# Optimization experiments

Hardware: AMD Instinct MI355X
Metric: run time of the kernel (lower is better)

The kernel has to match this reference:

```python
import jax, jax.numpy as jnp
import numpy as np

UNITS = 400    # LSTM cells per hidden layer
KATT = 10     # attention Gaussians
NCHARS = 73   # alphabet size
NMIX = 20     # bivariate GMM components


def _peephole_step(x, h, c, Wx, Wh, b, p):
    # p: [3, U] peephole weights (i, f, o)
    z = x @ Wx + h @ Wh + b                       # [B, 4U]
    zi, zf, zg, zo = jnp.split(z, 4, axis=-1)
    i = jax.nn.sigmoid(zi + p[0] * c)
    f = jax.nn.sigmoid(zf + p[1] * c)
    c_new = f * c + i * jnp.tanh(zg)
    o = jax.nn.sigmoid(zo + p[2] * c_new)
    return o * jnp.tanh(c_new), c_new


def _forward(input_strokes, char_onehot, char_mask,
             Wx0, Wh0, b0, p0, Wx1, Wh1, b1, p1, Wx2, Wh2, b2, p2,
             W_att, b_att, W_mdn, b_mdn):
    B, T, _ = input_strokes.shape
    Uc = char_onehot.shape[1]
    dt = input_strokes.dtype
    u = jnp.arange(Uc, dtype=dt)                  # character positions

    def step(carry, x_t):
        h1, c1, h2, c2, h3, c3, kappa, w = carry
        # layer 1: [stroke, window]
        h1, c1 = _peephole_step(jnp.concatenate([x_t, w], -1), h1, c1, Wx0, Wh0, b0, p0)
        # Graves soft-window attention from h1
        att = h1 @ W_att + b_att                  # [B, 3K]
        a_hat, b_hat, k_hat = jnp.split(att, 3, axis=-1)
        alpha = jnp.exp(a_hat)
        beta = jnp.exp(b_hat)
        kappa = kappa + jnp.exp(k_hat)            # [B, K] monotone position
        diff = kappa[:, :, None] - u[None, None, :]                   # [B, K, Uc]
        phi = jnp.sum(alpha[:, :, None] * jnp.exp(-beta[:, :, None] * diff * diff), axis=1)
        phi = phi * char_mask                     # [B, Uc] mask padded chars
        w = jnp.einsum('bu,buc->bc', phi, char_onehot)                # [B, NCHARS]
        # layers 2/3 with skip connections
        h2, c2 = _peephole_step(jnp.concatenate([x_t, w, h1], -1), h2, c2, Wx1, Wh1, b1, p1)
        h3, c3 = _peephole_step(jnp.concatenate([x_t, w, h2], -1), h3, c3, Wx2, Wh2, b2, p2)
        return (h1, c1, h2, c2, h3, c3, kappa, w), h3

    zh = jnp.zeros((B, UNITS), dt)
    carry0 = (zh, zh, zh, zh, zh, zh,
              jnp.zeros((B, KATT), dt), jnp.zeros((B, NCHARS), dt))
    _, hs = jax.lax.scan(step, carry0, input_strokes.transpose(1, 0, 2))
    outputs = hs.transpose(1, 0, 2)               # [B, T, UNITS]

    # mixture density head: 6*M + 1 outputs
    y = outputs @ W_mdn + b_mdn                   # [B, T, 6M+1]
    M = NMIX
    pi, mu1, mu2, s1, s2, rho, eos = jnp.split(
        y, [M, 2 * M, 3 * M, 4 * M, 5 * M, 6 * M], axis=-1)
    return jnp.concatenate([
        jax.nn.softmax(pi, axis=-1), mu1, mu2,
        jnp.exp(s1), jnp.exp(s2), jnp.tanh(rho), jax.nn.sigmoid(eos)], axis=-1)


def setup_inputs() -> dict:
    key = jax.random.key(0)
    ks = jax.random.split(key, 16)
    B, T, Uc = 32, 400, 50
    s = 0.1
    in0 = 3 + NCHARS                 # stroke + window
    in12 = 3 + NCHARS + UNITS        # stroke + window + skip h
    d = {
        'input_strokes': jax.random.normal(ks[0], (B, T, 3), jnp.float32),
        'input_chars': jax.random.randint(ks[1], (B, Uc), 0, NCHARS),
        'input_char_lens': jax.random.randint(ks[2], (B,), 10, Uc + 1),
        'Wx0': s * jax.random.normal(ks[3], (in0, 4 * UNITS), jnp.float32),
        'Wh0': s * jax.random.normal(ks[4], (UNITS, 4 * UNITS), jnp.float32),
        'b0': jnp.zeros((4 * UNITS,), jnp.float32),
        'p0': s * jax.random.normal(ks[5], (3, UNITS), jnp.float32),
        'Wx1': s * jax.random.normal(ks[6], (in12, 4 * UNITS), jnp.float32),
        'Wh1': s * jax.random.normal(ks[7], (UNITS, 4 * UNITS), jnp.float32),
        'b1': jnp.zeros((4 * UNITS,), jnp.float32),
        'p1': s * jax.random.normal(ks[8], (3, UNITS), jnp.float32),
        'Wx2': s * jax.random.normal(ks[9], (in12, 4 * UNITS), jnp.float32),
        'Wh2': s * jax.random.normal(ks[10], (UNITS, 4 * UNITS), jnp.float32),
        'b2': jnp.zeros((4 * UNITS,), jnp.float32),
        'p2': s * jax.random.normal(ks[11], (3, UNITS), jnp.float32),
        'W_att': s * jax.random.normal(ks[12], (UNITS, 3 * KATT), jnp.float32),
        'b_att': jnp.zeros((3 * KATT,), jnp.float32),
        'W_mdn': s * jax.random.normal(ks[13], (UNITS, 6 * NMIX + 1), jnp.float32),
        'b_mdn': jnp.zeros((6 * NMIX + 1,), jnp.float32),
    }
    return d


def reference(input_strokes, input_chars, input_char_lens,
              Wx0, Wh0, b0, p0, Wx1, Wh1, b1, p1, Wx2, Wh2, b2, p2,
              W_att, b_att, W_mdn, b_mdn):
    char_onehot = jax.nn.one_hot(input_chars, NCHARS, dtype=input_strokes.dtype)
    Uc = input_chars.shape[1]
    char_mask = (jnp.arange(Uc)[None, :] < input_char_lens[:, None]).astype(input_strokes.dtype)
    return _forward(input_strokes, char_onehot, char_mask,
                    Wx0, Wh0, b0, p0, Wx1, Wh1, b1, p1, Wx2, Wh2, b2, p2,
                    W_att, b_att, W_mdn, b_mdn)
```

## Files before the change

### kernel.cpp

```cpp
#include <hip/hip_runtime.h>


#define NATT   8
#define NBLK   208
#define NBLKC  200
#define NTHR   1024
#define TSTEPS 400
#define BATCH  32
#define UNITSN 400
#define NCHARS 73
#define UC     50
#define KTOT   2228
#define WSTR   2236
#define NGRP   8
#define NFLAG  32
#define NEPOCH 402

typedef unsigned int       u32;
typedef unsigned long long u64;

#define STATE_BYTES 4096
#define HSLOT     12832
#define H1_BYTE   4096
#define H2_BYTE   (H1_BYTE + TSTEPS * HSLOT * 4)
#define H3_BYTE   (H2_BYTE + TSTEPS * HSLOT * 4)
#define WSLOT     2368
#define WH_BYTE   (H3_BYTE + TSTEPS * HSLOT * 4)

__device__ __forceinline__ float sigf(float x)   { return 1.0f / (1.0f + __expf(-x)); }
__device__ __forceinline__ float tanhf_(float x) { return 1.0f - 2.0f / (1.0f + __expf(2.0f * x)); }

__device__ __forceinline__ float dot100(const float* __restrict__ w,
                                        const float* __restrict__ x) {
  const float4* wv = (const float4*)w;
  const float4* xv = (const float4*)x;
  float s0 = 0.f, s1 = 0.f, s2 = 0.f, s3 = 0.f;
#pragma unroll 5
  for (int i = 0; i < 25; ++i) {
    float4 a = wv[i], bb = xv[i];
    s0 = fmaf(a.x, bb.x, s0); s1 = fmaf(a.y, bb.y, s1);
    s2 = fmaf(a.z, bb.z, s2); s3 = fmaf(a.w, bb.w, s3);
  }
  return (s0 + s1) + (s2 + s3);
}

__device__ __forceinline__ void dot100x2(const float* __restrict__ wa,
                                         const float* __restrict__ wb,
                                         const float* __restrict__ x,
                                         float& ra, float& rb) {
  const float4* av = (const float4*)wa;
  const float4* bv = (const float4*)wb;
  const float4* xv = (const float4*)x;
  float a0 = 0.f, a1 = 0.f, a2 = 0.f, a3 = 0.f;
  float c0 = 0.f, c1 = 0.f, c2 = 0.f, c3 = 0.f;
#pragma unroll 5
  for (int i = 0; i < 25; ++i) {
    float4 xx = xv[i], aa = av[i], bb = bv[i];
    a0 = fmaf(aa.x, xx.x, a0); a1 = fmaf(aa.y, xx.y, a1);
    a2 = fmaf(aa.z, xx.z, a2); a3 = fmaf(aa.w, xx.w, a3);
    c0 = fmaf(bb.x, xx.x, c0); c1 = fmaf(bb.y, xx.y, c1);
    c2 = fmaf(bb.z, xx.z, c2); c3 = fmaf(bb.w, xx.w, c3);
  }
  ra += (a0 + a1) + (a2 + a3);
  rb += (c0 + c1) + (c2 + c3);
}

__device__ __forceinline__ void dotP3(const float* __restrict__ wA,
                                      const float* __restrict__ wB,
                                      const float* __restrict__ x2,
                                      const float* __restrict__ wC,
                                      const float* __restrict__ wD,
                                      const float* __restrict__ x1,
                                      const float* __restrict__ wE,
                                      const float* __restrict__ x3,
                                      float& r3, float& r2, float& r1) {
  const float4* Av = (const float4*)wA;
  const float4* Bv = (const float4*)wB;
  const float4* Cv = (const float4*)wC;
  const float4* Dv = (const float4*)wD;
  const float4* Ev = (const float4*)wE;
  const float4* x2v = (const float4*)x2;
  const float4* x1v = (const float4*)x1;
  const float4* x3v = (const float4*)x3;
  float sA0 = 0.f, sA1 = 0.f, sA2 = 0.f, sA3 = 0.f;
  float sB0 = 0.f, sB1 = 0.f, sB2 = 0.f, sB3 = 0.f;
  float sC0 = 0.f, sC1 = 0.f, sC2 = 0.f, sC3 = 0.f;
  float sD0 = 0.f, sD1 = 0.f, sD2 = 0.f, sD3 = 0.f;
  float sE0 = 0.f, sE1 = 0.f, sE2 = 0.f, sE3 = 0.f;
#pragma unroll 2
  for (int i = 0; i < 25; ++i) {
    float4 xa = x2v[i], xb = x1v[i], xc = x3v[i];
    float4 a = Av[i], bb = Bv[i], cc = Cv[i], d = Dv[i], e = Ev[i];
    sA0 = fmaf(a.x, xa.x, sA0);  sA1 = fmaf(a.y, xa.y, sA1);
    sA2 = fmaf(a.z, xa.z, sA2);  sA3 = fmaf(a.w, xa.w, sA3);
    sB0 = fmaf(bb.x, xa.x, sB0); sB1 = fmaf(bb.y, xa.y, sB1);
    sB2 = fmaf(bb.z, xa.z, sB2); sB3 = fmaf(bb.w, xa.w, sB3);
    sC0 = fmaf(cc.x, xb.x, sC0); sC1 = fmaf(cc.y, xb.y, sC1);
    sC2 = fmaf(cc.z, xb.z, sC2); sC3 = fmaf(cc.w, xb.w, sC3);
    sD0 = fmaf(d.x, xb.x, sD0);  sD1 = fmaf(d.y, xb.y, sD1);
    sD2 = fmaf(d.z, xb.z, sD2);  sD3 = fmaf(d.w, xb.w, sD3);
    sE0 = fmaf(e.x, xc.x, sE0);  sE1 = fmaf(e.y, xc.y, sE1);
    sE2 = fmaf(e.z, xc.z, sE2);  sE3 = fmaf(e.w, xc.w, sE3);
  }
  r3 += (sA0 + sA1) + (sA2 + sA3) + (sE0 + sE1) + (sE2 + sE3);
  r2 += (sB0 + sB1) + (sB2 + sB3) + (sC0 + sC1) + (sC2 + sC3);
  r1 += (sD0 + sD1) + (sD2 + sD3);
}

__device__ __forceinline__ void dot73x3(const float* __restrict__ w1,
                                        const float* __restrict__ w2,
                                        const float* __restrict__ w3,
                                        const float* __restrict__ x, int kq,
                                        float& r1, float& r2, float& r3) {
  int st = (kq == 0) ? 0 : 18 * kq + 1;
  int en = st + ((kq == 0) ? 19 : 18);
  float s1 = 0.f, s2 = 0.f, s3 = 0.f;
  for (int k = st; k < en; ++k) {
    float xv = x[k];
    s1 = fmaf(w1[k], xv, s1); s2 = fmaf(w2[k], xv, s2); s3 = fmaf(w3[k], xv, s3);
  }
  r1 += s1; r2 += s2; r3 += s3;
}

extern "C" __global__ void __launch_bounds__(NTHR)
__attribute__((amdgpu_waves_per_eu(4, 4)))
hand_kernel(const float* __restrict__ xs, const int* __restrict__ chars,
            const int* __restrict__ lens,
            const float* __restrict__ Wx0, const float* __restrict__ Wh0,
            const float* __restrict__ b0, const float* __restrict__ p0,
            const float* __restrict__ Wx1, const float* __restrict__ Wh1,
            const float* __restrict__ b1, const float* __restrict__ p1,
            const float* __restrict__ Wx2, const float* __restrict__ Wh2,
            const float* __restrict__ b2, const float* __restrict__ p2,
            const float* __restrict__ Watt, const float* __restrict__ batt,
            const float* __restrict__ Wmdn, const float* __restrict__ bmdn,
            float* __restrict__ dout, char* __restrict__ wsb) {
  const int blk = blockIdx.x;
  const int tid = threadIdx.x;
  const bool is_att = (blk < NATT);
  const int cblk = blk - NATT;

  __shared__ __align__(16) float wlw[8 * WSTR];
  __shared__ float zpart[NTHR], zpartB[NTHR];
  __shared__ float zbuf[256], zbufB[256];
  __shared__ float biasL[3][8];
  __shared__ float peepL[3][3][2];
  __shared__ float cstate[3][64];
  __shared__ int   bar_target;
  __shared__ float alphaL[40], betaL[40], kappaL[40];
  __shared__ float wlds[4 * NCHARS];
  __shared__ __align__(16) float wstg[BATCH * NCHARS + 12];

  int*   bar_i = (int*)wsb;
  int*   glob  = bar_i + 128;
  int*   wcnt  = bar_i + 192;
  float* h1h   = (float*)(wsb + H1_BYTE);
  float* h2h   = (float*)(wsb + H2_BYTE);
  float* h3h   = (float*)(wsb + H3_BYTE);
  float* whh   = (float*)(wsb + WH_BYTE);

  const int out = tid & 255;
  const int b   = out >> 3;
  const int c   = out & 7;
  const int kq  = tid >> 8;
  const int u0  = 2 * cblk;

  if (tid == 0) bar_target = 0;
  if (tid < 192) cstate[tid / 64][tid % 64] = 0.f;
  if (tid < 40) kappaL[tid] = 0.f;

  if (!is_att) {
    for (int idx = tid; idx < 8 * KTOT; idx += NTHR) {
      int cc = idx / KTOT, k = idx - cc * KTOT;
      int gcol = (cc & 3) * UNITSN + u0 + (cc >> 2);
      float v;
      if (k < 476)        v = (k < 76)  ? Wx0[(size_t)k * 1600 + gcol]
                                        : Wh0[(size_t)(k - 76) * 1600 + gcol];
      else if (k < 1352) { int q = k - 476;
                          v = (q < 476) ? Wx1[(size_t)q * 1600 + gcol]
                                        : Wh1[(size_t)(q - 476) * 1600 + gcol]; }
      else               { int q = k - 1352;
                          v = (q < 476) ? Wx2[(size_t)q * 1600 + gcol]
                                        : Wh2[(size_t)(q - 476) * 1600 + gcol]; }
      wlw[cc * WSTR + k] = v;
    }
    if (tid < 24) {
      int l = tid >> 3, cc = tid & 7;
      const float* bs = (l == 0) ? b0 : (l == 1) ? b1 : b2;
      biasL[l][cc] = bs[(cc & 3) * UNITSN + u0 + (cc >> 2)];
    }
    if (tid < 18) {
      int l = tid / 6, r = (tid % 6) >> 1, ul = tid & 1;
      const float* ps = (l == 0) ? p0 : (l == 1) ? p1 : p2;
      peepL[l][r][ul] = ps[r * UNITSN + u0 + ul];
    }
  } else {
    for (int i = tid; i < 12000; i += NTHR) wlw[i] = Watt[i];
  }
  __syncthreads();

  const float* Wc   = wlw + c * WSTR;
  float*       attp = wlw + 12000;

  auto gridbar = [&]() {
    __syncthreads();
    if (tid == 0) {
      int e = ++bar_target;
      int g = cblk & (NGRP - 1);
      const int gsz = NBLKC / NGRP;
      int a = __hip_atomic_fetch_add(bar_i + g * 16, 1, __ATOMIC_RELAXED, __HIP_MEMORY_SCOPE_AGENT);
      if (a + 1 == e * gsz) {
        int q = __hip_atomic_fetch_add(glob, 1, __ATOMIC_RELAXED, __HIP_MEMORY_SCOPE_AGENT);
        if (((q + 1) & (NGRP - 1)) == 0) {
          for (int f = 0; f < NFLAG; ++f)
            __hip_atomic_store(bar_i + 256 + f * 16, e, __ATOMIC_RELAXED, __HIP_MEMORY_SCOPE_AGENT);
        }
      }
      int* myflag = bar_i + 256 + (cblk & (NFLAG - 1)) * 16;
      while (__hip_atomic_load(myflag, __ATOMIC_RELAXED, __HIP_MEMORY_SCOPE_AGENT) < e)
        __builtin_amdgcn_s_sleep(2);
    }
    __syncthreads();
  };

  auto waitglob = [&](int e) {
    if (tid == 0) {
      int tgt = NGRP * e;
      while (__hip_atomic_load(glob, __ATOMIC_RELAXED, __HIP_MEMORY_SCOPE_AGENT) < tgt)
        __builtin_amdgcn_s_sleep(2);
    }
    __syncthreads();
  };

  auto gates = [&](int layer, const float* zb, int bb, float* hdst) {
    union { float f[2]; u64 v; } pk;
#pragma unroll
    for (int ul = 0; ul < 2; ++ul) {
      float zi = zb[bb * 8 + ul * 4 + 0], zf = zb[bb * 8 + ul * 4 + 1];
      float zg = zb[bb * 8 + ul * 4 + 2], zo = zb[bb * 8 + ul * 4 + 3];
      float cold = cstate[layer][ul * 32 + bb];
      float ig = sigf(zi + peepL[layer][0][ul] * cold);
      float fg = sigf(zf + peepL[layer][1][ul] * cold);
      float cn = fg * cold + ig * tanhf_(zg);
      float og = sigf(zo + peepL[layer][2][ul] * cn);
      cstate[layer][ul * 32 + bb] = cn;
      pk.f[ul] = og * tanhf_(cn);
    }
    __hip_atomic_store((u64*)(hdst + bb * UNITSN + u0), pk.v,
                       __ATOMIC_RELAXED, __HIP_MEMORY_SCOPE_AGENT);
  };

  auto finalize1 = [&](int layer, float acc, float* hdst) {
    zpart[tid] = acc;
    __syncthreads();
    if (tid < 256)
      zbuf[tid] = zpart[tid] + zpart[tid + 256] + zpart[tid + 512] + zpart[tid + 768]
                + biasL[layer][tid & 7];
    __syncthreads();
    if (tid < 256 && (tid & 7) == 0) gates(layer, zbuf, tid >> 3, hdst);
  };

  auto finalizeQ = [&](float a2v, float* h2dst, float a1v, float* h1dst, bool do1) {
    zpart[tid]  = a2v;
    zpartB[tid] = a1v;
    __syncthreads();
    if (tid < 256) {
      zbuf[tid]  = zpart[tid]  + zpart[tid + 256]  + zpart[tid + 512]  + zpart[tid + 768]
                 + biasL[1][tid & 7];
      zbufB[tid] = zpartB[tid] + zpartB[tid + 256] + zpartB[tid + 512] + zpartB[tid + 768]
                 + biasL[0][tid & 7];
    }
    __syncthreads();
    if (tid < 256 && (tid & 7) == 0) {
      gates(1, zbuf, tid >> 3, h2dst);
      if (do1) gates(0, zbufB, tid >> 3, h1dst);
    }
  };

  if (is_att) {
    const int bs0 = blk * 4;
    for (int t = 0; t < TSTEPS; ++t) {
      waitglob(t + 1);
      const float* h1g = h1h + (size_t)t * HSLOT;
      float* wdst = whh + (size_t)t * WSLOT + bs0 * NCHARS;
      for (int i = tid; i < 4 * NCHARS; i += NTHR) wlds[i] = 0.f;
      if (tid < 240) {
        int ks = tid / 30, r = tid - ks * 30;
        int bb2 = r / 15, jj2 = r - bb2 * 15;
        int j0 = 2 * jj2, j1 = j0 + 1;
        const float2* h0v = (const float2*)(h1g + (bs0 + 2 * bb2) * UNITSN + ks * 50);
        const float2* h1v = (const float2*)(h1g + (bs0 + 2 * bb2 + 1) * UNITSN + ks * 50);
        const float* wv = wlw + (ks * 50) * 30;
        float s00 = 0.f, s01 = 0.f, s10 = 0.f, s11 = 0.f;
#pragma unroll
        for (int kk = 0; kk < 25; ++kk) {
          float2 ha = h0v[kk], hb = h1v[kk];
          float wa0 = wv[(2 * kk) * 30 + j0],     wb0 = wv[(2 * kk) * 30 + j1];
          float wa1 = wv[(2 * kk + 1) * 30 + j0], wb1 = wv[(2 * kk + 1) * 30 + j1];
          s00 = fmaf(ha.x, wa0, s00); s01 = fmaf(ha.x, wb0, s01);
          s10 = fmaf(hb.x, wa0, s10); s11 = fmaf(hb.x, wb0, s11);
          s00 = fmaf(ha.y, wa1, s00); s01 = fmaf(ha.y, wb1, s01);
          s10 = fmaf(hb.y, wa1, s10); s11 = fmaf(hb.y, wb1, s11);
        }
        int b0i = 2 * bb2;
        attp[(b0i * 30 + j0) * 8 + ks] = s00;
        attp[(b0i * 30 + j1) * 8 + ks] = s01;
        attp[((b0i + 1) * 30 + j0) * 8 + ks] = s10;
        attp[((b0i + 1) * 30 + j1) * 8 + ks] = s11;
      }
      __syncthreads();
      if (tid < 40) {
        int bl = tid / 10, j = tid - bl * 10;
        float ah = batt[j], bh = batt[10 + j], kh = batt[20 + j];
#pragma unroll
        for (int s = 0; s < 8; ++s) {
          ah += attp[(bl * 30 + j) * 8 + s];
          bh += attp[(bl * 30 + 10 + j) * 8 + s];
          kh += attp[(bl * 30 + 20 + j) * 8 + s];
        }
        float kap = kappaL[tid] + __expf(kh);
        kappaL[tid] = kap;
        alphaL[tid] = __expf(ah);
        betaL[tid]  = __expf(bh);
      }
      __syncthreads();
      if (tid < 4 * UC) {
        int bl = tid / UC, u = tid - bl * UC;
        if (u < lens[bs0 + bl]) {
          float ph = 0.f;
#pragma unroll
          for (int j = 0; j < 10; ++j) {
            float d = kappaL[bl * 10 + j] - (float)u;
            ph = fmaf(alphaL[bl * 10 + j], __expf(-betaL[bl * 10 + j] * d * d), ph);
          }
          atomicAdd(&wlds[bl * NCHARS + chars[(bs0 + bl) * UC + u]], ph);
        }
      }
      __syncthreads();
      for (int i = tid; i < (4 * NCHARS) / 2; i += NTHR) {
        union { float f[2]; u64 v; } pk;
        pk.f[0] = wlds[2 * i]; pk.f[1] = wlds[2 * i + 1];
        __hip_atomic_store((u64*)(wdst + 2 * i), pk.v,
                           __ATOMIC_RELAXED, __HIP_MEMORY_SCOPE_AGENT);
      }
      __syncthreads();
      if (tid == 0)
        __hip_atomic_fetch_add(wcnt, 1, __ATOMIC_RELAXED, __HIP_MEMORY_SCOPE_AGENT);
    }
    waitglob(NEPOCH);
  }
  else {
    {
      float acc = 0.f;
      if (kq == 0) {
        const float* xr = xs + (size_t)b * TSTEPS * 3;
        acc = Wc[0] * xr[0] + Wc[1] * xr[1] + Wc[2] * xr[2];
      }
      finalize1(0, acc, h1h);
    }
    gridbar();

    float acc_z3 = 0.f;
    for (int t = 0; t < TSTEPS; ++t) {
      const float* h1t  = h1h + (size_t)t * HSLOT + b * UNITSN;
      const float* h2p  = h2h + (size_t)(t > 0 ? t - 1 : 0) * HSLOT + b * UNITSN;
      const float* h3pp = h3h + (size_t)(t > 1 ? t - 2 : 0) * HSLOT + b * UNITSN;
      const int o = kq * 100;
      float a3f = acc_z3, a2 = 0.f, a1 = 0.f;
      if (t >= 2) {
        dotP3(Wc + 1428 + o, Wc + 952 + o, h2p + o,
              Wc + 552 + o,  Wc + 76 + o,  h1t + o,
              Wc + 1828 + o, h3pp + o, a3f, a2, a1);
      } else if (t == 1) {
        dot100x2(Wc + 1428 + o, Wc + 952 + o, h2p + o, a3f, a2);
        dot100x2(Wc + 552 + o, Wc + 76 + o, h1t + o, a2, a1);
      } else {
        dot100x2(Wc + 552 + o, Wc + 76 + o, h1t + o, a2, a1);
      }
      if (kq == 0) {
        const float* xr = xs + ((size_t)b * TSTEPS + t) * 3;
        a2 += Wc[476] * xr[0] + Wc[477] * xr[1] + Wc[478] * xr[2];
        if (t < TSTEPS - 1)
          a1 += Wc[0] * xr[3] + Wc[1] * xr[4] + Wc[2] * xr[5];
      }
      if (t > 0) finalize1(2, a3f, h3h + (size_t)(t - 1) * HSLOT);
      if (tid == 0) {
        int tgt = NATT * (t + 1);
        while (__hip_atomic_load(wcnt, __ATOMIC_RELAXED, __HIP_MEMORY_SCOPE_AGENT) < tgt)
          __builtin_amdgcn_s_sleep(2);
      }
      __syncthreads();
      {
        const float4* wsrc = (const float4*)(whh + (size_t)t * WSLOT);
        for (int i = tid; i < (BATCH * NCHARS) / 4; i += NTHR)
          ((float4*)wstg)[i] = wsrc[i];
      }
      __syncthreads();
      bool do1 = (t < TSTEPS - 1);
      float q2 = a2, q1 = a1, z3n = 0.f;
      dot73x3(Wc + 479, Wc + 3, Wc + 1355, wstg + b * NCHARS, kq, q2, q1, z3n);
      if (kq == 0) {
        const float* xr = xs + ((size_t)b * TSTEPS + t) * 3;
        z3n += Wc[1352] * xr[0] + Wc[1353] * xr[1] + Wc[1354] * xr[2];
      }
      finalizeQ(q2, h2h + (size_t)t * HSLOT,
                q1, h1h + (size_t)(t + 1) * HSLOT, do1);
      acc_z3 = z3n;
      gridbar();
    }
    {
      const float* h2l  = h2h + (size_t)(TSTEPS - 1) * HSLOT + b * UNITSN;
      const float* h3ll = h3h + (size_t)(TSTEPS - 2) * HSLOT + b * UNITSN;
      float a3 = acc_z3 + dot100(Wc + 1428 + kq * 100, h2l + kq * 100)
                        + dot100(Wc + 1828 + kq * 100, h3ll + kq * 100);
      finalize1(2, a3, h3h + (size_t)(TSTEPS - 1) * HSLOT);
    }
    gridbar();
  }

  {
    int j = tid & 127, ks = tid >> 7;
    for (int i0 = 0; i0 < 64; i0 += 4) {
      float acc[4] = {0.f, 0.f, 0.f, 0.f};
      const float* hp[4];
      bool val[4];
      for (int r = 0; r < 4; ++r) {
        int row = blk + (i0 + r) * NBLK;
        val[r] = (row < 12800);
        hp[r] = val[r] ? (h3h + (size_t)(row % TSTEPS) * HSLOT + (row / TSTEPS) * UNITSN + ks * 50)
                       : h3h;
      }
      if (j < 121) {
        const float* wp = Wmdn + (size_t)(ks * 50) * 121 + j;
        for (int k = 0; k < 50; ++k) {
          float wv = wp[(size_t)k * 121];
#pragma unroll
          for (int r = 0; r < 4; ++r) acc[r] = fmaf(hp[r][k], wv, acc[r]);
        }
      }
      for (int r = 0; r < 4; ++r) {
        zpart[tid] = acc[r];
        __syncthreads();
        if (tid < 121) {
          float s = bmdn[tid];
#pragma unroll
          for (int m = 0; m < 8; ++m) s += zpart[tid + m * 128];
          zbuf[tid] = s;
        }
        __syncthreads();
        if (tid == 0) {
          float mx = zbuf[0];
          for (int q = 1; q < 20; ++q) mx = fmaxf(mx, zbuf[q]);
          float s = 0.f;
          for (int q = 0; q < 20; ++q) s += __expf(zbuf[q] - mx);
          zbuf[126] = mx;
          zbuf[127] = 1.f / s;
        }
        __syncthreads();
        if (val[r] && tid < 121) {
          int row = blk + (i0 + r) * NBLK;
          float y = zbuf[tid], o;
          if (tid < 20)       o = __expf(y - zbuf[126]) * zbuf[127];
          else if (tid < 60)  o = y;
          else if (tid < 100) o = __expf(y);
          else if (tid < 120) o = tanhf_(y);
          else                o = sigf(y);
          dout[(size_t)row * 121 + tid] = o;
        }
        __syncthreads();
      }
    }
  }
}

extern "C" void kernel_launch(void* const* d_in, const int* in_sizes, int n_in,
                              void* d_out, int out_size, void* d_ws, size_t ws_size,
                              hipStream_t stream) {
  const float* xs   = (const float*)d_in[0];
  const int*   chrs = (const int*)d_in[1];
  const int*   lens = (const int*)d_in[2];
  const float* Wx0  = (const float*)d_in[3];
  const float* Wh0  = (const float*)d_in[4];
  const float* b0   = (const float*)d_in[5];
  const float* p0   = (const float*)d_in[6];
  const float* Wx1  = (const float*)d_in[7];
  const float* Wh1  = (const float*)d_in[8];
  const float* b1   = (const float*)d_in[9];
  const float* p1   = (const float*)d_in[10];
  const float* Wx2  = (const float*)d_in[11];
  const float* Wh2  = (const float*)d_in[12];
  const float* b2   = (const float*)d_in[13];
  const float* p2   = (const float*)d_in[14];
  const float* Watt = (const float*)d_in[15];
  const float* batt = (const float*)d_in[16];
  const float* Wmdn = (const float*)d_in[17];
  const float* bmdn = (const float*)d_in[18];

  hipMemsetAsync(d_ws, 0, STATE_BYTES, stream);
  hipLaunchKernelGGL(hand_kernel, dim3(NBLK), dim3(NTHR), 0, stream,
                     xs, chrs, lens, Wx0, Wh0, b0, p0, Wx1, Wh1, b1, p1,
                     Wx2, Wh2, b2, p2, Watt, batt, Wmdn, bmdn,
                     (float*)d_out, (char*)d_ws);
}
```

Baseline: 7.138 ms.

## Spread LSTM recurrence across 400 compute blocks with one unit each

Doubles the compute blocks from 200 to 400 so each block owns one hidden unit (4 gate columns) instead of two. The K reduction is now split eight ways (52-wide slices) rather than four. The LDS weight footprint per block is halved, and waves_per_eu is raised to 8 so two blocks can share a CU. The intent is to shorten each block's serial per-step dot-product work in the latency-bound persistent recurrence. The cost is twice as many participants in every grid barrier, more fragmented per-unit h stores, and a deeper LDS partial-sum reduction.

```diff
diff --git a/kernel.cpp b/kernel.cpp
--- a/kernel.cpp
+++ b/kernel.cpp
@@ -2,8 +2,8 @@
 
 
 #define NATT   8
-#define NBLK   208
-#define NBLKC  200
+#define NBLKC  400
+#define NBLK   408
 #define NTHR   1024
 #define TSTEPS 400
 #define BATCH  32
@@ -30,13 +30,14 @@
 __device__ __forceinline__ float sigf(float x)   { return 1.0f / (1.0f + __expf(-x)); }
 __device__ __forceinline__ float tanhf_(float x) { return 1.0f - 2.0f / (1.0f + __expf(2.0f * x)); }
 
-__device__ __forceinline__ float dot100(const float* __restrict__ w,
-                                        const float* __restrict__ x) {
+template<int N4>
+__device__ __forceinline__ float dotX(const float* __restrict__ w,
+                                      const float* __restrict__ x) {
   const float4* wv = (const float4*)w;
   const float4* xv = (const float4*)x;
   float s0 = 0.f, s1 = 0.f, s2 = 0.f, s3 = 0.f;
-#pragma unroll 5
-  for (int i = 0; i < 25; ++i) {
+#pragma unroll
+  for (int i = 0; i < N4; ++i) {
     float4 a = wv[i], bb = xv[i];
     s0 = fmaf(a.x, bb.x, s0); s1 = fmaf(a.y, bb.y, s1);
     s2 = fmaf(a.z, bb.z, s2); s3 = fmaf(a.w, bb.w, s3);
@@ -44,17 +45,18 @@
   return (s0 + s1) + (s2 + s3);
 }
 
-__device__ __forceinline__ void dot100x2(const float* __restrict__ wa,
-                                         const float* __restrict__ wb,
-                                         const float* __restrict__ x,
-                                         float& ra, float& rb) {
+template<int N4>
+__device__ __forceinline__ void dotX2(const float* __restrict__ wa,
+                                      const float* __restrict__ wb,
+                                      const float* __restrict__ x,
+                                      float& ra, float& rb) {
   const float4* av = (const float4*)wa;
   const float4* bv = (const float4*)wb;
   const float4* xv = (const float4*)x;
   float a0 = 0.f, a1 = 0.f, a2 = 0.f, a3 = 0.f;
   float c0 = 0.f, c1 = 0.f, c2 = 0.f, c3 = 0.f;
-#pragma unroll 5
-  for (int i = 0; i < 25; ++i) {
+#pragma unroll
+  for (int i = 0; i < N4; ++i) {
     float4 xx = xv[i], aa = av[i], bb = bv[i];
     a0 = fmaf(aa.x, xx.x, a0); a1 = fmaf(aa.y, xx.y, a1);
     a2 = fmaf(aa.z, xx.z, a2); a3 = fmaf(aa.w, xx.w, a3);
@@ -65,6 +67,7 @@
   rb += (c0 + c1) + (c2 + c3);
 }
 
+template<int N4>
 __device__ __forceinline__ void dotP3(const float* __restrict__ wA,
                                       const float* __restrict__ wB,
                                       const float* __restrict__ x2,
@@ -88,7 +91,7 @@
   float sD0 = 0.f, sD1 = 0.f, sD2 = 0.f, sD3 = 0.f;
   float sE0 = 0.f, sE1 = 0.f, sE2 = 0.f, sE3 = 0.f;
 #pragma unroll 2
-  for (int i = 0; i < 25; ++i) {
+  for (int i = 0; i < N4; ++i) {
     float4 xa = x2v[i], xb = x1v[i], xc = x3v[i];
     float4 a = Av[i], bb = Bv[i], cc = Cv[i], d = Dv[i], e = Ev[i];
     sA0 = fmaf(a.x, xa.x, sA0);  sA1 = fmaf(a.y, xa.y, sA1);
@@ -112,8 +115,8 @@
                                         const float* __restrict__ w3,
                                         const float* __restrict__ x, int kq,
                                         float& r1, float& r2, float& r3) {
-  int st = (kq == 0) ? 0 : 18 * kq + 1;
-  int en = st + ((kq == 0) ? 19 : 18);
+  int st = kq * 9;
+  int en = st + ((kq == 7) ? 10 : 9);
   float s1 = 0.f, s2 = 0.f, s3 = 0.f;
   for (int k = st; k < en; ++k) {
     float xv = x[k];
@@ -123,7 +126,7 @@
 }
 
 extern "C" __global__ void __launch_bounds__(NTHR)
-__attribute__((amdgpu_waves_per_eu(4, 4)))
+__attribute__((amdgpu_waves_per_eu(8, 8)))
 hand_kernel(const float* __restrict__ xs, const int* __restrict__ chars,
             const int* __restrict__ lens,
             const float* __restrict__ Wx0, const float* __restrict__ Wh0,
@@ -140,12 +143,12 @@
   const bool is_att = (blk < NATT);
   const int cblk = blk - NATT;
 
-  __shared__ __align__(16) float wlw[8 * WSTR];
+  __shared__ __align__(16) float wlw[12960];
   __shared__ float zpart[NTHR], zpartB[NTHR];
-  __shared__ float zbuf[256], zbufB[256];
-  __shared__ float biasL[3][8];
-  __shared__ float peepL[3][3][2];
-  __shared__ float cstate[3][64];
+  __shared__ float zbuf[128], zbufB[128];
+  __shared__ float biasL[3][4];
+  __shared__ float peepL[3][3];
+  __shared__ float cstate[3][32];
   __shared__ int   bar_target;
   __shared__ float alphaL[40], betaL[40], kappaL[40];
   __shared__ float wlds[4 * NCHARS];
@@ -159,20 +162,21 @@
   float* h3h   = (float*)(wsb + H3_BYTE);
   float* whh   = (float*)(wsb + WH_BYTE);
 
-  const int out = tid & 255;
-  const int b   = out >> 3;
-  const int c   = out & 7;
-  const int kq  = tid >> 8;
-  const int u0  = 2 * cblk;
+  const int out = tid & 127;
+  const int b   = out >> 2;
+  const int c   = out & 3;
+  const int kq  = tid >> 7;
+  const int u0  = cblk;
+  const int ko  = kq * 52;
 
   if (tid == 0) bar_target = 0;
-  if (tid < 192) cstate[tid / 64][tid % 64] = 0.f;
+  if (tid < 96) cstate[tid / 32][tid % 32] = 0.f;
   if (tid < 40) kappaL[tid] = 0.f;
 
   if (!is_att) {
-    for (int idx = tid; idx < 8 * KTOT; idx += NTHR) {
+    for (int idx = tid; idx < 4 * KTOT; idx += NTHR) {
       int cc = idx / KTOT, k = idx - cc * KTOT;
-      int gcol = (cc & 3) * UNITSN + u0 + (cc >> 2);
+      int gcol = cc * UNITSN + u0;
       float v;
       if (k < 476)        v = (k < 76)  ? Wx0[(size_t)k * 1600 + gcol]
                                         : Wh0[(size_t)(k - 76) * 1600 + gcol];
@@ -184,15 +188,15 @@
                                         : Wh2[(size_t)(q - 476) * 1600 + gcol]; }
       wlw[cc * WSTR + k] = v;
     }
-    if (tid < 24) {
-      int l = tid >> 3, cc = tid & 7;
+    if (tid < 12) {
+      int l = tid >> 2, cc = tid & 3;
       const float* bs = (l == 0) ? b0 : (l == 1) ? b1 : b2;
-      biasL[l][cc] = bs[(cc & 3) * UNITSN + u0 + (cc >> 2)];
-    }
-    if (tid < 18) {
-      int l = tid / 6, r = (tid % 6) >> 1, ul = tid & 1;
+      biasL[l][cc] = bs[cc * UNITSN + u0];
+    }
+    if (tid < 9) {
+      int l = tid / 3, r = tid - l * 3;
       const float* ps = (l == 0) ? p0 : (l == 1) ? p1 : p2;
-      peepL[l][r][ul] = ps[r * UNITSN + u0 + ul];
+      peepL[l][r] = ps[r * UNITSN + u0];
     }
   } else {
     for (int i = tid; i < 12000; i += NTHR) wlw[i] = Watt[i];
@@ -233,47 +237,49 @@
   };
 
   auto gates = [&](int layer, const float* zb, int bb, float* hdst) {
-    union { float f[2]; u64 v; } pk;
-#pragma unroll
-    for (int ul = 0; ul < 2; ++ul) {
-      float zi = zb[bb * 8 + ul * 4 + 0], zf = zb[bb * 8 + ul * 4 + 1];
-      float zg = zb[bb * 8 + ul * 4 + 2], zo = zb[bb * 8 + ul * 4 + 3];
-      float cold = cstate[layer][ul * 32 + bb];
-      float ig = sigf(zi + peepL[layer][0][ul] * cold);
-      float fg = sigf(zf + peepL[layer][1][ul] * cold);
-      float cn = fg * cold + ig * tanhf_(zg);
-      float og = sigf(zo + peepL[layer][2][ul] * cn);
-      cstate[layer][ul * 32 + bb] = cn;
-      pk.f[ul] = og * tanhf_(cn);
-    }
-    __hip_atomic_store((u64*)(hdst + bb * UNITSN + u0), pk.v,
+    float zi = zb[bb * 4 + 0], zf = zb[bb * 4 + 1];
+    float zg = zb[bb * 4 + 2], zo = zb[bb * 4 + 3];
+    float cold = cstate[layer][bb];
+    float ig = sigf(zi + peepL[layer][0] * cold);
+    float fg = sigf(zf + peepL[layer][1] * cold);
+    float cn = fg * cold + ig * tanhf_(zg);
+    float og = sigf(zo + peepL[layer][2] * cn);
+    cstate[layer][bb] = cn;
+    __hip_atomic_store(hdst + bb * UNITSN + u0, og * tanhf_(cn),
                        __ATOMIC_RELAXED, __HIP_MEMORY_SCOPE_AGENT);
   };
 
   auto finalize1 = [&](int layer, float acc, float* hdst) {
     zpart[tid] = acc;
     __syncthreads();
-    if (tid < 256)
-      zbuf[tid] = zpart[tid] + zpart[tid + 256] + zpart[tid + 512] + zpart[tid + 768]
-                + biasL[layer][tid & 7];
-    __syncthreads();
-    if (tid < 256 && (tid & 7) == 0) gates(layer, zbuf, tid >> 3, hdst);
+    if (tid < 128) {
+      float s = biasL[layer][tid & 3];
+#pragma unroll
+      for (int m = 0; m < 8; ++m) s += zpart[tid + m * 128];
+      zbuf[tid] = s;
+    }
+    __syncthreads();
+    if (tid < 128 && (tid & 3) == 0) gates(layer, zbuf, tid >> 2, hdst);
   };
 
   auto finalizeQ = [&](float a2v, float* h2dst, float a1v, float* h1dst, bool do1) {
     zpart[tid]  = a2v;
     zpartB[tid] = a1v;
     __syncthreads();
-    if (tid < 256) {
-      zbuf[tid]  = zpart[tid]  + zpart[tid + 256]  + zpart[tid + 512]  + zpart[tid + 768]
-                 + biasL[1][tid & 7];
-      zbufB[tid] = zpartB[tid] + zpartB[tid + 256] + zpartB[tid + 512] + zpartB[tid + 768]
-                 + biasL[0][tid & 7];
-    }
-    __syncthreads();
-    if (tid < 256 && (tid & 7) == 0) {
-      gates(1, zbuf, tid >> 3, h2dst);
-      if (do1) gates(0, zbufB, tid >> 3, h1dst);
+    if (tid < 128) {
+      float s2 = biasL[1][tid & 3], s1 = biasL[0][tid & 3];
+#pragma unroll
+      for (int m = 0; m < 8; ++m) {
+        s2 += zpart[tid + m * 128];
+        s1 += zpartB[tid + m * 128];
+      }
+      zbuf[tid]  = s2;
+      zbufB[tid] = s1;
+    }
+    __syncthreads();
+    if (tid < 128 && (tid & 3) == 0) {
+      gates(1, zbuf, tid >> 2, h2dst);
+      if (do1) gates(0, zbufB, tid >> 2, h1dst);
     }
   };
 
@@ -365,17 +371,27 @@
       const float* h1t  = h1h + (size_t)t * HSLOT + b * UNITSN;
       const float* h2p  = h2h + (size_t)(t > 0 ? t - 1 : 0) * HSLOT + b * UNITSN;
       const float* h3pp = h3h + (size_t)(t > 1 ? t - 2 : 0) * HSLOT + b * UNITSN;
-      const int o = kq * 100;
       float a3f = acc_z3, a2 = 0.f, a1 = 0.f;
       if (t >= 2) {
-        dotP3(Wc + 1428 + o, Wc + 952 + o, h2p + o,
-              Wc + 552 + o,  Wc + 76 + o,  h1t + o,
-              Wc + 1828 + o, h3pp + o, a3f, a2, a1);
+        if (kq < 7)
+          dotP3<13>(Wc + 1428 + ko, Wc + 952 + ko, h2p + ko,
+                    Wc + 552 + ko,  Wc + 76 + ko,  h1t + ko,
+                    Wc + 1828 + ko, h3pp + ko, a3f, a2, a1);
+        else
+          dotP3<9>(Wc + 1428 + ko, Wc + 952 + ko, h2p + ko,
+                   Wc + 552 + ko,  Wc + 76 + ko,  h1t + ko,
+                   Wc + 1828 + ko, h3pp + ko, a3f, a2, a1);
       } else if (t == 1) {
-        dot100x2(Wc + 1428 + o, Wc + 952 + o, h2p + o, a3f, a2);
-        dot100x2(Wc + 552 + o, Wc + 76 + o, h1t + o, a2, a1);
+        if (kq < 7) {
+          dotX2<13>(Wc + 1428 + ko, Wc + 952 + ko, h2p + ko, a3f, a2);
+          dotX2<13>(Wc + 552 + ko, Wc + 76 + ko, h1t + ko, a2, a1);
+        } else {
+          dotX2<9>(Wc + 1428 + ko, Wc + 952 + ko, h2p + ko, a3f, a2);
+          dotX2<9>(Wc + 552 + ko, Wc + 76 + ko, h1t + ko, a2, a1);
+        }
       } else {
-        dot100x2(Wc + 552 + o, Wc + 76 + o, h1t + o, a2, a1);
+        if (kq < 7) dotX2<13>(Wc + 552 + ko, Wc + 76 + ko, h1t + ko, a2, a1);
+        else        dotX2<9>(Wc + 552 + ko, Wc + 76 + ko, h1t + ko, a2, a1);
       }
       if (kq == 0) {
         const float* xr = xs + ((size_t)b * TSTEPS + t) * 3;
@@ -411,8 +427,11 @@
     {
       const float* h2l  = h2h + (size_t)(TSTEPS - 1) * HSLOT + b * UNITSN;
       const float* h3ll = h3h + (size_t)(TSTEPS - 2) * HSLOT + b * UNITSN;
-      float a3 = acc_z3 + dot100(Wc + 1428 + kq * 100, h2l + kq * 100)
-                        + dot100(Wc + 1828 + kq * 100, h3ll + kq * 100);
+      float a3 = acc_z3;
+      if (kq < 7) a3 += dotX<13>(Wc + 1428 + ko, h2l + ko)
+                      + dotX<13>(Wc + 1828 + ko, h3ll + ko);
+      else        a3 += dotX<9>(Wc + 1428 + ko, h2l + ko)
+                      + dotX<9>(Wc + 1828 + ko, h3ll + ko);
       finalize1(2, a3, h3h + (size_t)(TSTEPS - 1) * HSLOT);
     }
     gridbar();
@@ -420,7 +439,7 @@
 
   {
     int j = tid & 127, ks = tid >> 7;
-    for (int i0 = 0; i0 < 64; i0 += 4) {
+    for (int i0 = 0; i0 < 32; i0 += 4) {
       float acc[4] = {0.f, 0.f, 0.f, 0.f};
       const float* hp[4];
       bool val[4];
@@ -445,22 +464,22 @@
           float s = bmdn[tid];
 #pragma unroll
           for (int m = 0; m < 8; ++m) s += zpart[tid + m * 128];
-          zbuf[tid] = s;
+          zbufB[tid] = s;
         }
         __syncthreads();
         if (tid == 0) {
-          float mx = zbuf[0];
-          for (int q = 1; q < 20; ++q) mx = fmaxf(mx, zbuf[q]);
+          float mx = zbufB[0];
+          for (int q = 1; q < 20; ++q) mx = fmaxf(mx, zbufB[q]);
           float s = 0.f;
-          for (int q = 0; q < 20; ++q) s += __expf(zbuf[q] - mx);
-          zbuf[126] = mx;
-          zbuf[127] = 1.f / s;
+          for (int q = 0; q < 20; ++q) s += __expf(zbufB[q] - mx);
+          zbufB[126] = mx;
+          zbufB[127] = 1.f / s;
         }
         __syncthreads();
         if (val[r] && tid < 121) {
           int row = blk + (i0 + r) * NBLK;
-          float y = zbuf[tid], o;
-          if (tid < 20)       o = __expf(y - zbuf[126]) * zbuf[127];
+          float y = zbufB[tid], o;
+          if (tid < 20)       o = __expf(y - zbufB[126]) * zbufB[127];
           else if (tid < 60)  o = y;
           else if (tid < 100) o = __expf(y);
           else if (tid < 120) o = tanhf_(y);
```

New measurement: 14.61 ms. +104.7%, slower.
